# Performance work log

Measured on AMD Instinct MI355X. Metric: run time of the kernel, lower is better.

The kernel has to match this reference:

```python
import jax, jax.numpy as jnp
import numpy as np

B, N, F_IN, F_OUT, H = 4, 2048, 64, 64, 4

def setup_inputs() -> dict:
    key = jax.random.key(0)
    k1, k2, k3, k4 = jax.random.split(key, 4)
    node_features = jax.random.normal(k1, (B, N, F_IN), dtype=jnp.float32)
    adj_matrix = jax.random.randint(k2, (B, N, N), 0, 2, dtype=jnp.int32)
    # nn.Linear(in, H*out, bias=False): stored here as [in, H*out] so y = x @ W
    W = jax.random.normal(k3, (F_IN, H * F_OUT), dtype=jnp.float32) * (1.0 / np.sqrt(F_IN))
    # per-head additive-attention vector over concatenated [h_i || h_j] (width 2*F_OUT)
    attention = jax.random.normal(k4, (H, 2 * F_OUT), dtype=jnp.float32) * 0.1
    return {"node_features": node_features, "adj_matrix": adj_matrix, "W": W, "attention": attention}

def reference(node_features, adj_matrix, W, attention):
    Bv, Nv = node_features.shape[0], node_features.shape[1]
    # h: [B, H, N, F_OUT]
    h = (node_features @ W).reshape(Bv, Nv, H, F_OUT).transpose(0, 2, 1, 3)
    # Additive GAT scores: a_h . [h_i || h_j] decomposed so the [B,H,N,N,2F] concat
    # tensor is never materialized (same math as concat + einsum in the source).
    a_src, a_dst = attention[:, :F_OUT], attention[:, F_OUT:]
    s_src = jnp.einsum('bhnf,hf->bhn', h, a_src)
    s_dst = jnp.einsum('bhnf,hf->bhn', h, a_dst)
    scores = s_src[:, :, :, None] + s_dst[:, :, None, :]          # [B,H,N,N]
    scores = jnp.where(scores >= 0, scores, 0.2 * scores)          # LeakyReLU(0.2)
    mask = adj_matrix[:, None, :, :].astype(bool)                  # [B,1,N,N]
    scores = jnp.where(mask, scores, -jnp.inf)                     # masked_fill(~mask, -inf)
    attn = jax.nn.softmax(scores, axis=-1)                         # softmax over neighbors j
    # dropout is identity in eval mode (deterministic reference)
    h_prime = jnp.einsum('bhij,bhjf->bhif', attn, h)               # weighted neighbor sum
    return h_prime.transpose(0, 2, 1, 3).reshape(Bv, Nv, H * F_OUT)
```

## Files before the change

### kernel.cpp

```cpp
#include <hip/hip_runtime.h>

#define NN 2048
#define NH 4
#define COLS 256

typedef __attribute__((ext_vector_type(8))) short short8;
typedef __attribute__((ext_vector_type(4))) float f32x4;
typedef __attribute__((ext_vector_type(4))) int i32x4;
typedef __attribute__((ext_vector_type(4))) unsigned u32x4;

__device__ __forceinline__ unsigned cvtpk(float lo, float hi) {
  unsigned r;
  asm("v_cvt_pk_bf16_f32 %0, %1, %2" : "=v"(r) : "v"(lo), "v"(hi));
  return r;
}
__device__ __forceinline__ unsigned pack16(i32x4 a, i32x4 b, i32x4 c, i32x4 d) {
  unsigned m = 0;
  #pragma unroll
  for (int e = 0; e < 4; ++e) {
    m |= (a[e] != 0 ? 1u : 0u) << e;
    m |= (b[e] != 0 ? 1u : 0u) << (e + 4);
    m |= (c[e] != 0 ? 1u : 0u) << (e + 8);
    m |= (d[e] != 0 ? 1u : 0u) << (e + 12);
  }
  return m;
}

#define ONES8 {(short)0x3F80, (short)0x3F80, (short)0x3F80, (short)0x3F80, \
               (short)0x3F80, (short)0x3F80, (short)0x3F80, (short)0x3F80}

__global__ __launch_bounds__(256) void k1_prep(
    const float* __restrict__ nf, const float* __restrict__ W,
    const float* __restrict__ att, ushort* __restrict__ hB,
    float* __restrict__ s_src, float* __restrict__ s_dst)
{
  const int tid = threadIdx.x;
  const int head = tid >> 6, lane = tid & 63;
  const int bid = blockIdx.x;
  const int m0 = bid * 8;

  float w[64];
  #pragma unroll
  for (int f = 0; f < 64; ++f) w[f] = W[f * COLS + tid];

  const float LOG2E = 1.4426950408889634f;
  const float asrc = att[head * 128 + lane] * LOG2E;
  const float adst = att[head * 128 + 64 + lane] * LOG2E;

  __shared__ float xs[512];
  xs[tid]       = nf[m0 * 64 + tid];
  xs[tid + 256] = nf[m0 * 64 + 256 + tid];
  __syncthreads();

  float hv[8];
  #pragma unroll
  for (int rr = 0; rr < 8; ++rr) {
    float acc = 0.f;
    #pragma unroll
    for (int f = 0; f < 64; ++f) acc = fmaf(xs[rr * 64 + f], w[f], acc);
    hv[rr] = acc;
    float vs = acc * asrc, vd = acc * adst;
    #pragma unroll
    for (int off = 32; off > 0; off >>= 1) {
      vs += __shfl_xor(vs, off);
      vd += __shfl_xor(vd, off);
    }
    if (lane == 0) {
      const int m = m0 + rr;
      const int b = m >> 11, n = m & (NN - 1);
      s_src[(b * NH + head) * NN + n] = vs;
      s_dst[(b * NH + head) * NN + n] = vd;
    }
  }

  const int b   = m0 >> 11;
  const int n0  = m0 & (NN - 1);
  const int jc  = n0 >> 5;
  const int grp = (n0 >> 3) & 3;
  const int t   = (tid >> 4) & 3, fl = tid & 15;
  uint4 vv;
  vv.x = cvtpk(hv[0], hv[1]);
  vv.y = cvtpk(hv[2], hv[3]);
  vv.z = cvtpk(hv[4], hv[5]);
  vv.w = cvtpk(hv[6], hv[7]);
  const size_t chunk =
      (((size_t)(b * NH + head) * 64 + jc) * 4 + t) * 64 + (grp * 16 + fl);
  *(uint4*)(hB + chunk * 8) = vv;
}

__global__ __launch_bounds__(256) void k2_main(
    const int* __restrict__ adj, const ushort* __restrict__ hB,
    const float* __restrict__ s_src, const float* __restrict__ s_dst,
    float* __restrict__ out)
{
  const int tid = threadIdx.x;
  const int h   = tid >> 6;
  const int l   = tid & 63;
  const int L   = blockIdx.x;
  const int xcd  = L & 7, pos = L >> 3;
  const int b    = xcd >> 1;
  const int iblk = (xcd & 1) * 64 + pos;
  const int i0   = iblk << 4;
  const int bh   = b * NH + h;
  const int r16  = l & 15;
  const int grp  = l >> 4;
  const int koff = grp << 3;

  __shared__ float    sdl[NH * NN];
  __shared__ unsigned abits[16][65];

  {
    const int srow = tid >> 4, sseg = tid & 15;
    const int* sb = adj + ((size_t)(b * NN + i0 + srow)) * NN + sseg * 128;
    #pragma unroll
    for (int p = 0; p < 4; ++p) {
      const i32x4 a0 = *(const i32x4*)(sb + p * 32);
      const i32x4 a1 = *(const i32x4*)(sb + p * 32 + 4);
      const i32x4 a2 = *(const i32x4*)(sb + p * 32 + 8);
      const i32x4 a3 = *(const i32x4*)(sb + p * 32 + 12);
      const i32x4 a4 = *(const i32x4*)(sb + p * 32 + 16);
      const i32x4 a5 = *(const i32x4*)(sb + p * 32 + 20);
      const i32x4 a6 = *(const i32x4*)(sb + p * 32 + 24);
      const i32x4 a7 = *(const i32x4*)(sb + p * 32 + 28);
      abits[srow][sseg * 4 + p] = pack16(a0, a1, a2, a3) | (pack16(a4, a5, a6, a7) << 16);
    }
  }
  {
    const float* sp = s_dst + (size_t)b * NH * NN;
    #pragma unroll
    for (int k = 0; k < 8; ++k) {
      const int di = k * 1024 + tid * 4;
      *(f32x4*)&sdl[di] = *(const f32x4*)(sp + di);
    }
  }
  __syncthreads();

  const float ssl = s_src[bh * NN + i0 + r16];
  const ushort* hbSrc = hB + (size_t)bh * 131072 + l * 8;
  const short8 ones = ONES8;
  const float* sdh = &sdl[h * NN];

  f32x4 acc[4];
  #pragma unroll
  for (int q = 0; q < 4; ++q) acc[q] = (f32x4){0.f, 0.f, 0.f, 0.f};
  f32x4 acd = (f32x4){0.f, 0.f, 0.f, 0.f};

#define LOADQ(D0, D1, D2, D3, JC)                          \
  D0 = *(const short8*)(hbSrc + (JC) * 2048);              \
  D1 = *(const short8*)(hbSrc + (JC) * 2048 + 512);        \
  D2 = *(const short8*)(hbSrc + (JC) * 2048 + 1024);       \
  D3 = *(const short8*)(hbSrc + (JC) * 2048 + 1536);       \
  asm volatile("" : "+v"(D0), "+v"(D1), "+v"(D2), "+v"(D3));

  short8 c0, c1, c2, c3, n0, n1, n2, n3;
  LOADQ(c0, c1, c2, c3, 0);
  LOADQ(n0, n1, n2, n3, 1);

  #pragma unroll 1
  for (int jc = 0; jc < 64; ++jc) {
    const int jp = (jc + 2 < 64) ? jc + 2 : 63;
    short8 m0, m1, m2, m3;
    LOADQ(m0, m1, m2, m3, jp);

    const int jb = jc * 32 + koff;
    const f32x4 sd0 = *(const f32x4*)(sdh + jb);
    const f32x4 sd1 = *(const f32x4*)(sdh + jb + 4);
    const unsigned msk = abits[r16][jc] >> koff;

    float pl[8];
    #pragma unroll
    for (int e = 0; e < 8; ++e) {
      const float sdv = (e < 4) ? sd0[e] : sd1[e - 4];
      float x = ssl + sdv;
      x = fmaxf(x, 0.2f * x);
      const float p = __builtin_amdgcn_exp2f(x);
      pl[e] = ((msk >> e) & 1u) ? p : 0.f;
    }
    u32x4 pa;
    #pragma unroll
    for (int e2 = 0; e2 < 4; ++e2) pa[e2] = cvtpk(pl[2 * e2], pl[2 * e2 + 1]);
    union { u32x4 u; short8 s; } ca; ca.u = pa;
    const short8 pal = ca.s;

    acc[0] = __builtin_amdgcn_mfma_f32_16x16x32_bf16(pal, c0, acc[0], 0, 0, 0);
    acc[1] = __builtin_amdgcn_mfma_f32_16x16x32_bf16(pal, c1, acc[1], 0, 0, 0);
    acc[2] = __builtin_amdgcn_mfma_f32_16x16x32_bf16(pal, c2, acc[2], 0, 0, 0);
    acc[3] = __builtin_amdgcn_mfma_f32_16x16x32_bf16(pal, c3, acc[3], 0, 0, 0);
    acd    = __builtin_amdgcn_mfma_f32_16x16x32_bf16(pal, ones, acd,   0, 0, 0);

    c0 = n0; c1 = n1; c2 = n2; c3 = n3;
    n0 = m0; n1 = m1; n2 = m2; n3 = m3;
  }
#undef LOADQ

  float rl[4];
  #pragma unroll
  for (int r = 0; r < 4; ++r) rl[r] = 1.0f / acd[r];
  #pragma unroll
  for (int t = 0; t < 4; ++t) {
    #pragma unroll
    for (int r = 0; r < 4; ++r) {
      const int i = i0 + grp * 4 + r;
      const size_t oidx = ((size_t)(b * NN + i) * COLS) + h * 64 + t * 16 + r16;
      out[oidx] = acc[t][r] * rl[r];
    }
  }
}

extern "C" void kernel_launch(void* const* d_in, const int* in_sizes, int n_in,
                              void* d_out, int out_size, void* d_ws, size_t ws_size,
                              hipStream_t stream) {
  const float* nf  = (const float*)d_in[0];
  const int*   adj = (const int*)d_in[1];
  const float* W   = (const float*)d_in[2];
  const float* att = (const float*)d_in[3];

  ushort* hB    = (ushort*)d_ws;
  float*  s_src = (float*)((char*)d_ws + (size_t)16 * 64 * NN * 2);
  float*  s_dst = s_src + 16 * NN;

  hipLaunchKernelGGL(k1_prep, dim3(1024), dim3(256), 0, stream,
                     nf, W, att, hB, s_src, s_dst);
  hipLaunchKernelGGL(k2_main, dim3(512), dim3(256), 0, stream,
                     adj, hB, s_src, s_dst, (float*)d_out);
}
```

Measured before the change: 64.03 us.

## Double row tile, split neighbor range across waves, stage h via LDS

Each block now handles 32 rows with 512 threads. Two waves per head each take half of the neighbor range and combine their partial sums through LDS at the end. The h tiles are streamed into a triple-buffered LDS ring with global_load_lds, and each h fragment feeds two row tiles, which halves h traffic per row. The cost is larger LDS use, fewer blocks (256) and a reduction step. The adjacency staging assumes 512 threads cover 32 rows, which matches the new layout.

```diff
diff --git a/kernel.cpp b/kernel.cpp
--- a/kernel.cpp
+++ b/kernel.cpp
@@ -24,6 +24,11 @@
     m |= (d[e] != 0 ? 1u : 0u) << (e + 12);
   }
   return m;
+}
+__device__ __forceinline__ void gload_lds16(const void* g, void* l) {
+  __builtin_amdgcn_global_load_lds(
+      (const __attribute__((address_space(1))) void*)g,
+      (__attribute__((address_space(3))) void*)l, 16, 0, 0);
 }
 
 #define ONES8 {(short)0x3F80, (short)0x3F80, (short)0x3F80, (short)0x3F80, \
@@ -88,26 +93,29 @@
   *(uint4*)(hB + chunk * 8) = vv;
 }
 
-__global__ __launch_bounds__(256) void k2_main(
+__global__ __launch_bounds__(512) void k2_main(
     const int* __restrict__ adj, const ushort* __restrict__ hB,
     const float* __restrict__ s_src, const float* __restrict__ s_dst,
     float* __restrict__ out)
 {
   const int tid = threadIdx.x;
-  const int h   = tid >> 6;
+  const int wv  = tid >> 6;
+  const int h   = wv >> 1;
+  const int js  = wv & 1;
   const int l   = tid & 63;
   const int L   = blockIdx.x;
-  const int xcd  = L & 7, pos = L >> 3;
-  const int b    = xcd >> 1;
-  const int iblk = (xcd & 1) * 64 + pos;
-  const int i0   = iblk << 4;
+  const int xcd = L & 7;
+  const int b   = xcd >> 1;
+  const int iblk = (xcd & 1) * 32 + (L >> 3);
+  const int i0   = iblk << 5;
   const int bh   = b * NH + h;
   const int r16  = l & 15;
   const int grp  = l >> 4;
   const int koff = grp << 3;
 
+  __shared__ ushort   hbuf[NH][2][3][2048];
   __shared__ float    sdl[NH * NN];
-  __shared__ unsigned abits[16][65];
+  __shared__ unsigned abits[32][65];
 
   {
     const int srow = tid >> 4, sseg = tid & 15;
@@ -128,81 +136,135 @@
   {
     const float* sp = s_dst + (size_t)b * NH * NN;
     #pragma unroll
-    for (int k = 0; k < 8; ++k) {
-      const int di = k * 1024 + tid * 4;
+    for (int k = 0; k < 4; ++k) {
+      const int di = k * 2048 + tid * 4;
       *(f32x4*)&sdl[di] = *(const f32x4*)(sp + di);
     }
   }
   __syncthreads();
 
-  const float ssl = s_src[bh * NN + i0 + r16];
+  const float ssl0 = s_src[bh * NN + i0 + r16];
+  const float ssl1 = s_src[bh * NN + i0 + 16 + r16];
   const ushort* hbSrc = hB + (size_t)bh * 131072 + l * 8;
+  const float* sdh = &sdl[h * NN];
   const short8 ones = ONES8;
-  const float* sdh = &sdl[h * NN];
-
-  f32x4 acc[4];
-  #pragma unroll
-  for (int q = 0; q < 4; ++q) acc[q] = (f32x4){0.f, 0.f, 0.f, 0.f};
-  f32x4 acd = (f32x4){0.f, 0.f, 0.f, 0.f};
-
-#define LOADQ(D0, D1, D2, D3, JC)                          \
-  D0 = *(const short8*)(hbSrc + (JC) * 2048);              \
-  D1 = *(const short8*)(hbSrc + (JC) * 2048 + 512);        \
-  D2 = *(const short8*)(hbSrc + (JC) * 2048 + 1024);       \
-  D3 = *(const short8*)(hbSrc + (JC) * 2048 + 1536);       \
-  asm volatile("" : "+v"(D0), "+v"(D1), "+v"(D2), "+v"(D3));
-
-  short8 c0, c1, c2, c3, n0, n1, n2, n3;
-  LOADQ(c0, c1, c2, c3, 0);
-  LOADQ(n0, n1, n2, n3, 1);
-
+  const int base = js * 32;
+
+  f32x4 acc[8];
+  #pragma unroll
+  for (int q = 0; q < 8; ++q) acc[q] = (f32x4){0.f, 0.f, 0.f, 0.f};
+  f32x4 acd0 = (f32x4){0.f, 0.f, 0.f, 0.f};
+  f32x4 acd1 = (f32x4){0.f, 0.f, 0.f, 0.f};
+
+#define STAGE(BUF, JC)                                                     \
+  {                                                                        \
+    _Pragma("unroll")                                                      \
+    for (int t = 0; t < 4; ++t)                                            \
+      gload_lds16(hbSrc + (size_t)(JC) * 2048 + t * 512,                   \
+                  &hbuf[h][js][(BUF)][t * 512]);                           \
+  }
+
+#define BODY(JCL, BUF, DO_STAGE)                                           \
+  {                                                                        \
+    const int jcg = base + (JCL);                                          \
+    const short8 hb0 = *(const short8*)&hbuf[h][js][(BUF)][l * 8];         \
+    const short8 hb1 = *(const short8*)&hbuf[h][js][(BUF)][512 + l * 8];   \
+    const short8 hb2 = *(const short8*)&hbuf[h][js][(BUF)][1024 + l * 8];  \
+    const short8 hb3 = *(const short8*)&hbuf[h][js][(BUF)][1536 + l * 8];  \
+    const int jb = jcg * 32 + koff;                                        \
+    const f32x4 sd0 = *(const f32x4*)(sdh + jb);                           \
+    const f32x4 sd1 = *(const f32x4*)(sdh + jb + 4);                       \
+    const unsigned msk0 = abits[r16][jcg] >> koff;                         \
+    const unsigned msk1 = abits[r16 + 16][jcg] >> koff;                    \
+    asm volatile("s_waitcnt lgkmcnt(0)" ::: "memory");                     \
+    __builtin_amdgcn_sched_barrier(0);                                     \
+    if (DO_STAGE) STAGE((BUF), jcg + 3);                                   \
+    float pl0[8], pl1[8];                                                  \
+    _Pragma("unroll")                                                      \
+    for (int e = 0; e < 8; ++e) {                                          \
+      const float sdv = (e < 4) ? sd0[e] : sd1[e - 4];                     \
+      float x = ssl0 + sdv;                                                \
+      x = fmaxf(x, 0.2f * x);                                              \
+      const float p = __builtin_amdgcn_exp2f(x);                           \
+      pl0[e] = ((msk0 >> e) & 1u) ? p : 0.f;                               \
+      float y = ssl1 + sdv;                                                \
+      y = fmaxf(y, 0.2f * y);                                              \
+      const float q = __builtin_amdgcn_exp2f(y);                           \
+      pl1[e] = ((msk1 >> e) & 1u) ? q : 0.f;                               \
+    }                                                                      \
+    u32x4 pa, pb;                                                          \
+    _Pragma("unroll")                                                      \
+    for (int e2 = 0; e2 < 4; ++e2) {                                       \
+      pa[e2] = cvtpk(pl0[2 * e2], pl0[2 * e2 + 1]);                        \
+      pb[e2] = cvtpk(pl1[2 * e2], pl1[2 * e2 + 1]);                        \
+    }                                                                      \
+    union { u32x4 u; short8 s; } ca, cb; ca.u = pa; cb.u = pb;             \
+    const short8 pal0 = ca.s, pal1 = cb.s;                                 \
+    acc[0] = __builtin_amdgcn_mfma_f32_16x16x32_bf16(pal0, hb0, acc[0], 0, 0, 0); \
+    acc[1] = __builtin_amdgcn_mfma_f32_16x16x32_bf16(pal0, hb1, acc[1], 0, 0, 0); \
+    acc[2] = __builtin_amdgcn_mfma_f32_16x16x32_bf16(pal0, hb2, acc[2], 0, 0, 0); \
+    acc[3] = __builtin_amdgcn_mfma_f32_16x16x32_bf16(pal0, hb3, acc[3], 0, 0, 0); \
+    acd0   = __builtin_amdgcn_mfma_f32_16x16x32_bf16(pal0, ones, acd0,    0, 0, 0); \
+    acc[4] = __builtin_amdgcn_mfma_f32_16x16x32_bf16(pal1, hb0, acc[4], 0, 0, 0); \
+    acc[5] = __builtin_amdgcn_mfma_f32_16x16x32_bf16(pal1, hb1, acc[5], 0, 0, 0); \
+    acc[6] = __builtin_amdgcn_mfma_f32_16x16x32_bf16(pal1, hb2, acc[6], 0, 0, 0); \
+    acc[7] = __builtin_amdgcn_mfma_f32_16x16x32_bf16(pal1, hb3, acc[7], 0, 0, 0); \
+    acd1   = __builtin_amdgcn_mfma_f32_16x16x32_bf16(pal1, ones, acd1,    0, 0, 0); \
+  }
+
+  STAGE(0, base);
+  STAGE(1, base + 1);
+  STAGE(2, base + 2);
+
+  int buf = 0;
   #pragma unroll 1
-  for (int jc = 0; jc < 64; ++jc) {
-    const int jp = (jc + 2 < 64) ? jc + 2 : 63;
-    short8 m0, m1, m2, m3;
-    LOADQ(m0, m1, m2, m3, jp);
-
-    const int jb = jc * 32 + koff;
-    const f32x4 sd0 = *(const f32x4*)(sdh + jb);
-    const f32x4 sd1 = *(const f32x4*)(sdh + jb + 4);
-    const unsigned msk = abits[r16][jc] >> koff;
-
-    float pl[8];
-    #pragma unroll
-    for (int e = 0; e < 8; ++e) {
-      const float sdv = (e < 4) ? sd0[e] : sd1[e - 4];
-      float x = ssl + sdv;
-      x = fmaxf(x, 0.2f * x);
-      const float p = __builtin_amdgcn_exp2f(x);
-      pl[e] = ((msk >> e) & 1u) ? p : 0.f;
-    }
-    u32x4 pa;
-    #pragma unroll
-    for (int e2 = 0; e2 < 4; ++e2) pa[e2] = cvtpk(pl[2 * e2], pl[2 * e2 + 1]);
-    union { u32x4 u; short8 s; } ca; ca.u = pa;
-    const short8 pal = ca.s;
-
-    acc[0] = __builtin_amdgcn_mfma_f32_16x16x32_bf16(pal, c0, acc[0], 0, 0, 0);
-    acc[1] = __builtin_amdgcn_mfma_f32_16x16x32_bf16(pal, c1, acc[1], 0, 0, 0);
-    acc[2] = __builtin_amdgcn_mfma_f32_16x16x32_bf16(pal, c2, acc[2], 0, 0, 0);
-    acc[3] = __builtin_amdgcn_mfma_f32_16x16x32_bf16(pal, c3, acc[3], 0, 0, 0);
-    acd    = __builtin_amdgcn_mfma_f32_16x16x32_bf16(pal, ones, acd,   0, 0, 0);
-
-    c0 = n0; c1 = n1; c2 = n2; c3 = n3;
-    n0 = m0; n1 = m1; n2 = m2; n3 = m3;
-  }
-#undef LOADQ
-
-  float rl[4];
-  #pragma unroll
-  for (int r = 0; r < 4; ++r) rl[r] = 1.0f / acd[r];
-  #pragma unroll
-  for (int t = 0; t < 4; ++t) {
-    #pragma unroll
-    for (int r = 0; r < 4; ++r) {
-      const int i = i0 + grp * 4 + r;
-      const size_t oidx = ((size_t)(b * NN + i) * COLS) + h * 64 + t * 16 + r16;
-      out[oidx] = acc[t][r] * rl[r];
+  for (int jcL = 0; jcL < 29; ++jcL) {
+    asm volatile("s_waitcnt vmcnt(8)" ::: "memory");
+    BODY(jcL, buf, 1);
+    buf = (buf == 2) ? 0 : buf + 1;
+  }
+  asm volatile("s_waitcnt vmcnt(8)" ::: "memory");
+  BODY(29, buf, 0);
+  buf = (buf == 2) ? 0 : buf + 1;
+  asm volatile("s_waitcnt vmcnt(4)" ::: "memory");
+  BODY(30, buf, 0);
+  buf = (buf == 2) ? 0 : buf + 1;
+  asm volatile("s_waitcnt vmcnt(0)" ::: "memory");
+  BODY(31, buf, 0);
+#undef BODY
+#undef STAGE
+
+  __syncthreads();
+  f32x4* red = (f32x4*)&hbuf[0][0][0][0];
+  if (js) {
+    #pragma unroll
+    for (int q = 0; q < 8; ++q) red[(h * 10 + q) * 64 + l] = acc[q];
+    red[(h * 10 + 8) * 64 + l] = acd0;
+    red[(h * 10 + 9) * 64 + l] = acd1;
+  }
+  __syncthreads();
+
+  if (!js) {
+    #pragma unroll
+    for (int q = 0; q < 8; ++q) acc[q] += red[(h * 10 + q) * 64 + l];
+    acd0 += red[(h * 10 + 8) * 64 + l];
+    acd1 += red[(h * 10 + 9) * 64 + l];
+
+    float rl[2][4];
+    #pragma unroll
+    for (int r = 0; r < 4; ++r) { rl[0][r] = 1.0f / acd0[r]; rl[1][r] = 1.0f / acd1[r]; }
+    #pragma unroll
+    for (int s = 0; s < 2; ++s) {
+      #pragma unroll
+      for (int t = 0; t < 4; ++t) {
+        const f32x4 a = acc[s * 4 + t];
+        #pragma unroll
+        for (int r = 0; r < 4; ++r) {
+          const int i = i0 + s * 16 + grp * 4 + r;
+          const size_t oidx = ((size_t)(b * NN + i) * COLS) + h * 64 + t * 16 + r16;
+          out[oidx] = a[r] * rl[s][r];
+        }
+      }
     }
   }
 }
@@ -221,6 +283,6 @@
 
   hipLaunchKernelGGL(k1_prep, dim3(1024), dim3(256), 0, stream,
                      nf, W, att, hB, s_src, s_dst);
-  hipLaunchKernelGGL(k2_main, dim3(512), dim3(256), 0, stream,
+  hipLaunchKernelGGL(k2_main, dim3(256), dim3(512), 0, stream,
                      adj, hB, s_src, s_dst, (float*)d_out);
 }
```

Result: faster. 56.33 us (-12.0%).
